# Kernel tuning notes

Measured on AMD Instinct MI355X. Metric: run time of the kernel, lower is better.

## Reference

```python
import jax, jax.numpy as jnp
import numpy as np

BATCH = 32768


def _unpack(packed, n):
    # packed: [rows, ceil(n/8)] ints in [0,256). Extract bits MSB-first per byte.
    bits = (packed[:, :, None] >> jnp.arange(7, -1, -1, dtype=packed.dtype)) & 1
    return bits.reshape(packed.shape[0], -1)[:, :n]  # [rows, n] of {0,1}


def setup_inputs() -> dict:
    key = jax.random.key(0)
    k0, k1, k2, k3, k4 = jax.random.split(key, 5)
    return {
        "x": jax.random.normal(k0, (BATCH, 784), dtype=jnp.float32),
        "w1_packed": jax.random.randint(k1, (256, 98), 0, 256, dtype=jnp.int32),
        "m1_packed": jax.random.randint(k2, (256, 98), 0, 256, dtype=jnp.int32),
        "alpha1": jnp.float32(1.0),
        "w2_packed": jax.random.randint(k3, (10, 32), 0, 256, dtype=jnp.int32),
        "m2_packed": jax.random.randint(k4, (10, 32), 0, 256, dtype=jnp.int32),
        "alpha2": jnp.float32(1.0),
    }


def reference(x, w1_packed, m1_packed, alpha1, w2_packed, m2_packed, alpha2):
    # Layer 1: binary {-1,+1} weights * {0,1} mask * alpha
    w1 = (2 * _unpack(w1_packed, 784) - 1).astype(jnp.float32)
    w1 = w1 * _unpack(m1_packed, 784).astype(jnp.float32) * alpha1  # [256, 784]
    h = jax.nn.relu(jnp.einsum('bi,oi->bo', x, w1))  # [B, 256]
    # Layer 2
    w2 = (2 * _unpack(w2_packed, 256) - 1).astype(jnp.float32)
    w2 = w2 * _unpack(m2_packed, 256).astype(jnp.float32) * alpha2  # [10, 256]
    return jnp.einsum('bh,oh->bo', h, w2)  # [B, 10]
```

## Files before the change

### kernel.cpp

```cpp
#include <hip/hip_runtime.h>
#include <hip/hip_bf16.h>

typedef __bf16 bf16x8 __attribute__((ext_vector_type(8)));
typedef float floatx4 __attribute__((ext_vector_type(4)));

__device__ __forceinline__ unsigned short f2bf(float f) {
  __bf16 b = (__bf16)f;
  return __builtin_bit_cast(unsigned short, b);
}

__global__ void decode_w1_kernel(const int* __restrict__ w1p,
                                 const int* __restrict__ m1p,
                                 unsigned short* __restrict__ w1t) {
  int t = blockIdx.x * 256 + threadIdx.x;
  int r = t & 255;
  int j = t >> 8;
  unsigned short vals[8];
#pragma unroll
  for (int k = 0; k < 8; ++k) vals[k] = 0;
  if (j < 98) {
    unsigned int v = (unsigned int)w1p[r * 98 + j];
    unsigned int m = (unsigned int)m1p[r * 98 + j];
#pragma unroll
    for (int k = 0; k < 8; ++k) {
      unsigned int bit = (v >> (7 - k)) & 1u;
      unsigned int mk  = (m >> (7 - k)) & 1u;
      vals[k] = (unsigned short)(mk ? (bit ? 0x3F80u : 0xBF80u) : 0u);
    }
  }
  uint4 pack;
  pack.x = (unsigned)vals[0] | ((unsigned)vals[1] << 16);
  pack.y = (unsigned)vals[2] | ((unsigned)vals[3] << 16);
  pack.z = (unsigned)vals[4] | ((unsigned)vals[5] << 16);
  pack.w = (unsigned)vals[6] | ((unsigned)vals[7] << 16);
  *reinterpret_cast<uint4*>(w1t + t * 8) = pack;
}

#define BM 64
#define NCHG 26
#define NCHP 13
#define HS_LD 264
#define W2_LD 264

#define OFF_W2 16896

__global__ __launch_bounds__(512, 4) void fused_kernel(
    const float* __restrict__ x,
    const unsigned short* __restrict__ w1t,
    const int* __restrict__ w2p,
    const int* __restrict__ m2p,
    const float* __restrict__ a1p,
    const float* __restrict__ a2p,
    float* __restrict__ out) {
  __shared__ unsigned short smem[26624];

  const int tid  = threadIdx.x;
  const int wave = tid >> 6;
  const int lane = tid & 63;
  const int l15  = lane & 15;
  const int quad = lane >> 4;
  const int row0 = blockIdx.x * BM;

  floatx4 acc[4][2];
#pragma unroll
  for (int i = 0; i < 4; ++i)
#pragma unroll
    for (int j = 0; j < 2; ++j) acc[i][j] = (floatx4){0.f, 0.f, 0.f, 0.f};

  const unsigned short* wl = w1t + ((size_t)wave * 32 + l15) * 8;

  auto ldfrags = [&](int cg, int cl, bf16x8* af, bf16x8* bfv) {
#pragma unroll
    for (int mi = 0; mi < 4; ++mi)
      af[mi] = *reinterpret_cast<const bf16x8*>(
          &smem[((cl * 4 + quad) * 64 + mi * 16 + l15) * 8]);
#pragma unroll
    for (int nj = 0; nj < 2; ++nj)
      bfv[nj] = *reinterpret_cast<const bf16x8*>(
          wl + (size_t)(cg * 4 + quad) * 2048 + nj * 128);
  };
  auto mm = [&](bf16x8* af, bf16x8* bfv) {
#pragma unroll
    for (int mi = 0; mi < 4; ++mi)
#pragma unroll
      for (int nj = 0; nj < 2; ++nj)
        acc[mi][nj] = __builtin_amdgcn_mfma_f32_16x16x32_bf16(
            af[mi], bfv[nj], acc[mi][nj], 0, 0, 0);
  };

  auto superphase = [&](const int sp) {
    const int r  = tid >> 3;
    const int g0 = tid & 7;
    {
      float4 xv[7];
#pragma unroll
      for (int it = 0; it < 7; ++it) {
        int g = g0 + it * 8;
        int col = sp * 416 + g * 4;
        if (col < 784)
          xv[it] = *reinterpret_cast<const float4*>(
              x + (size_t)(row0 + r) * 784 + col);
        else
          xv[it] = (float4){0.f, 0.f, 0.f, 0.f};
      }
#pragma unroll
      for (int it = 0; it < 7; ++it) {
        int g = g0 + it * 8;
        ushort4 b;
        b.x = f2bf(xv[it].x); b.y = f2bf(xv[it].y);
        b.z = f2bf(xv[it].z); b.w = f2bf(xv[it].w);
        *reinterpret_cast<ushort4*>(&smem[((g >> 1) * 64 + r) * 8 + (g & 1) * 4]) = b;
      }
    }
    {
      float4 xv[6];
#pragma unroll
      for (int it = 0; it < 6; ++it) {
        int g = g0 + 56 + it * 8;
        int col = sp * 416 + g * 4;
        if (col < 784)
          xv[it] = *reinterpret_cast<const float4*>(
              x + (size_t)(row0 + r) * 784 + col);
        else
          xv[it] = (float4){0.f, 0.f, 0.f, 0.f};
      }
#pragma unroll
      for (int it = 0; it < 6; ++it) {
        int g = g0 + 56 + it * 8;
        ushort4 b;
        b.x = f2bf(xv[it].x); b.y = f2bf(xv[it].y);
        b.z = f2bf(xv[it].z); b.w = f2bf(xv[it].w);
        *reinterpret_cast<ushort4*>(&smem[((g >> 1) * 64 + r) * 8 + (g & 1) * 4]) = b;
      }
    }
    __syncthreads();

    bf16x8 afA[4], bfA[2], afB[4], bfB[2];
    ldfrags(sp * NCHP, 0, afA, bfA);
#pragma unroll
    for (int cl = 0; cl < NCHP; ++cl) {
      if ((cl & 1) == 0) {
        if (cl < NCHP - 1) ldfrags(sp * NCHP + cl + 1, cl + 1, afB, bfB);
        mm(afA, bfA);
      } else {
        if (cl < NCHP - 1) ldfrags(sp * NCHP + cl + 1, cl + 1, afA, bfA);
        mm(afB, bfB);
      }
    }
    __syncthreads();
  };

  superphase(0);
  superphase(1);

  const float a1 = a1p[0];
  const float a2 = a2p[0];
#pragma unroll
  for (int mi = 0; mi < 4; ++mi) {
#pragma unroll
    for (int nj = 0; nj < 2; ++nj) {
      int col   = wave * 32 + nj * 16 + l15;
      int rbase = mi * 16 + quad * 4;
#pragma unroll
      for (int r = 0; r < 4; ++r) {
        float h = fmaxf(a1 * acc[mi][nj][r], 0.f);
        smem[(rbase + r) * HS_LD + col] = f2bf(h);
      }
    }
  }
  if (tid < 320) {
    int r = tid >> 5, j = tid & 31;
    unsigned int v = (unsigned int)w2p[r * 32 + j];
    unsigned int m = (unsigned int)m2p[r * 32 + j];
#pragma unroll
    for (int k = 0; k < 8; ++k) {
      unsigned int bit = (v >> (7 - k)) & 1u;
      unsigned int mk  = (m >> (7 - k)) & 1u;
      smem[OFF_W2 + r * W2_LD + j * 8 + k] =
          (unsigned short)(mk ? (bit ? 0x3F80u : 0xBF80u) : 0u);
    }
  }
  for (int idx = tid; idx < 6 * 256; idx += 512) {
    int r = 10 + (idx >> 8), c = idx & 255;
    smem[OFF_W2 + r * W2_LD + c] = 0;
  }
  __syncthreads();

  if (wave < 4) {
    floatx4 o2 = (floatx4){0.f, 0.f, 0.f, 0.f};
#pragma unroll
    for (int ks = 0; ks < 8; ++ks) {
      bf16x8 ha = *reinterpret_cast<const bf16x8*>(
          &smem[(wave * 16 + l15) * HS_LD + ks * 32 + quad * 8]);
      bf16x8 wb = *reinterpret_cast<const bf16x8*>(
          &smem[OFF_W2 + l15 * W2_LD + ks * 32 + quad * 8]);
      o2 = __builtin_amdgcn_mfma_f32_16x16x32_bf16(ha, wb, o2, 0, 0, 0);
    }
    if (l15 < 10) {
#pragma unroll
      for (int r = 0; r < 4; ++r) {
        int gr = row0 + wave * 16 + quad * 4 + r;
        out[(size_t)gr * 10 + l15] = a2 * o2[r];
      }
    }
  }
}

extern "C" void kernel_launch(void* const* d_in, const int* in_sizes, int n_in,
                              void* d_out, int out_size, void* d_ws, size_t ws_size,
                              hipStream_t stream) {
  const float* x   = (const float*)d_in[0];
  const int*   w1p = (const int*)d_in[1];
  const int*   m1p = (const int*)d_in[2];
  const float* a1  = (const float*)d_in[3];
  const int*   w2p = (const int*)d_in[4];
  const int*   m2p = (const int*)d_in[5];
  const float* a2  = (const float*)d_in[6];
  unsigned short* w1t = (unsigned short*)d_ws;
  float* out = (float*)d_out;

  decode_w1_kernel<<<104, 256, 0, stream>>>(w1p, m1p, w1t);
  fused_kernel<<<512, 512, 0, stream>>>(x, w1t, w2p, m2p, a1, a2, out);
}
```

Before: 170.9 us.

## Halve row tile to 32 and load full x row block in one pass

```diff
diff --git a/kernel.cpp b/kernel.cpp
--- a/kernel.cpp
+++ b/kernel.cpp
@@ -36,13 +36,12 @@
   *reinterpret_cast<uint4*>(w1t + t * 8) = pack;
 }
 
-#define BM 64
+#define BM 32
 #define NCHG 26
-#define NCHP 13
 #define HS_LD 264
 #define W2_LD 264
 
-#define OFF_W2 16896
+#define OFF_W2 8448
 
 __global__ __launch_bounds__(512, 4) void fused_kernel(
     const float* __restrict__ x,
@@ -61,102 +60,63 @@
   const int quad = lane >> 4;
   const int row0 = blockIdx.x * BM;
 
-  floatx4 acc[4][2];
+  {
+    const int r  = tid >> 4;
+    const int g0 = tid & 15;
+    float4 xv[13];
 #pragma unroll
-  for (int i = 0; i < 4; ++i)
+    for (int it = 0; it < 13; ++it) {
+      int g = g0 + it * 16;
+      int col = g * 4;
+      if (col < 784)
+        xv[it] = *reinterpret_cast<const float4*>(
+            x + (size_t)(row0 + r) * 784 + col);
+      else
+        xv[it] = (float4){0.f, 0.f, 0.f, 0.f};
+    }
+#pragma unroll
+    for (int it = 0; it < 13; ++it) {
+      int g = g0 + it * 16;
+      ushort4 b;
+      b.x = f2bf(xv[it].x); b.y = f2bf(xv[it].y);
+      b.z = f2bf(xv[it].z); b.w = f2bf(xv[it].w);
+      *reinterpret_cast<ushort4*>(&smem[(g >> 1) * 256 + r * 8 + (g & 1) * 4]) = b;
+    }
+  }
+  __syncthreads();
+
+  floatx4 acc[2][2];
+#pragma unroll
+  for (int i = 0; i < 2; ++i)
 #pragma unroll
     for (int j = 0; j < 2; ++j) acc[i][j] = (floatx4){0.f, 0.f, 0.f, 0.f};
 
   const unsigned short* wl = w1t + ((size_t)wave * 32 + l15) * 8;
 
-  auto ldfrags = [&](int cg, int cl, bf16x8* af, bf16x8* bfv) {
 #pragma unroll
-    for (int mi = 0; mi < 4; ++mi)
+  for (int cl = 0; cl < NCHG; ++cl) {
+    bf16x8 af[2], bfv[2];
+#pragma unroll
+    for (int mi = 0; mi < 2; ++mi)
       af[mi] = *reinterpret_cast<const bf16x8*>(
-          &smem[((cl * 4 + quad) * 64 + mi * 16 + l15) * 8]);
+          &smem[(cl * 4 + quad) * 256 + (mi * 16 + l15) * 8]);
 #pragma unroll
     for (int nj = 0; nj < 2; ++nj)
       bfv[nj] = *reinterpret_cast<const bf16x8*>(
-          wl + (size_t)(cg * 4 + quad) * 2048 + nj * 128);
-  };
-  auto mm = [&](bf16x8* af, bf16x8* bfv) {
+          wl + (size_t)(cl * 4 + quad) * 2048 + nj * 128);
 #pragma unroll
-    for (int mi = 0; mi < 4; ++mi)
+    for (int mi = 0; mi < 2; ++mi)
 #pragma unroll
       for (int nj = 0; nj < 2; ++nj)
         acc[mi][nj] = __builtin_amdgcn_mfma_f32_16x16x32_bf16(
             af[mi], bfv[nj], acc[mi][nj], 0, 0, 0);
-  };
-
-  auto superphase = [&](const int sp) {
-    const int r  = tid >> 3;
-    const int g0 = tid & 7;
-    {
-      float4 xv[7];
-#pragma unroll
-      for (int it = 0; it < 7; ++it) {
-        int g = g0 + it * 8;
-        int col = sp * 416 + g * 4;
-        if (col < 784)
-          xv[it] = *reinterpret_cast<const float4*>(
-              x + (size_t)(row0 + r) * 784 + col);
-        else
-          xv[it] = (float4){0.f, 0.f, 0.f, 0.f};
-      }
-#pragma unroll
-      for (int it = 0; it < 7; ++it) {
-        int g = g0 + it * 8;
-        ushort4 b;
-        b.x = f2bf(xv[it].x); b.y = f2bf(xv[it].y);
-        b.z = f2bf(xv[it].z); b.w = f2bf(xv[it].w);
-        *reinterpret_cast<ushort4*>(&smem[((g >> 1) * 64 + r) * 8 + (g & 1) * 4]) = b;
-      }
-    }
-    {
-      float4 xv[6];
-#pragma unroll
-      for (int it = 0; it < 6; ++it) {
-        int g = g0 + 56 + it * 8;
-        int col = sp * 416 + g * 4;
-        if (col < 784)
-          xv[it] = *reinterpret_cast<const float4*>(
-              x + (size_t)(row0 + r) * 784 + col);
-        else
-          xv[it] = (float4){0.f, 0.f, 0.f, 0.f};
-      }
-#pragma unroll
-      for (int it = 0; it < 6; ++it) {
-        int g = g0 + 56 + it * 8;
-        ushort4 b;
-        b.x = f2bf(xv[it].x); b.y = f2bf(xv[it].y);
-        b.z = f2bf(xv[it].z); b.w = f2bf(xv[it].w);
-        *reinterpret_cast<ushort4*>(&smem[((g >> 1) * 64 + r) * 8 + (g & 1) * 4]) = b;
-      }
-    }
-    __syncthreads();
-
-    bf16x8 afA[4], bfA[2], afB[4], bfB[2];
-    ldfrags(sp * NCHP, 0, afA, bfA);
-#pragma unroll
-    for (int cl = 0; cl < NCHP; ++cl) {
-      if ((cl & 1) == 0) {
-        if (cl < NCHP - 1) ldfrags(sp * NCHP + cl + 1, cl + 1, afB, bfB);
-        mm(afA, bfA);
-      } else {
-        if (cl < NCHP - 1) ldfrags(sp * NCHP + cl + 1, cl + 1, afA, bfA);
-        mm(afB, bfB);
-      }
-    }
-    __syncthreads();
-  };
-
-  superphase(0);
-  superphase(1);
+  }
+  __syncthreads();
 
   const float a1 = a1p[0];
   const float a2 = a2p[0];
 #pragma unroll
-  for (int mi = 0; mi < 4; ++mi) {
+  for (int mi = 0; mi < 2; ++mi) {
 #pragma unroll
     for (int nj = 0; nj < 2; ++nj) {
       int col   = wave * 32 + nj * 16 + l15;
@@ -186,7 +146,7 @@
   }
   __syncthreads();
 
-  if (wave < 4) {
+  if (wave < 2) {
     floatx4 o2 = (floatx4){0.f, 0.f, 0.f, 0.f};
 #pragma unroll
     for (int ks = 0; ks < 8; ++ks) {
@@ -220,5 +180,5 @@
   float* out = (float*)d_out;
 
   decode_w1_kernel<<<104, 256, 0, stream>>>(w1p, m1p, w1t);
-  fused_kernel<<<512, 512, 0, stream>>>(x, w1t, w2p, m2p, a1, a2, out);
+  fused_kernel<<<1024, 512, 0, stream>>>(x, w1t, w2p, m2p, a1, a2, out);
 }
```

After: 172.4 us. About the same (+0.9%).

## Overlap second-half x loads with first-half MFMA compute in fused MLP kernel

Applied to the files above, without the earlier changes.

```diff
diff --git a/kernel.cpp b/kernel.cpp
--- a/kernel.cpp
+++ b/kernel.cpp
@@ -37,8 +37,6 @@
 }
 
 #define BM 64
-#define NCHG 26
-#define NCHP 13
 #define HS_LD 264
 #define W2_LD 264
 
@@ -69,89 +67,108 @@
 
   const unsigned short* wl = w1t + ((size_t)wave * 32 + l15) * 8;
 
-  auto ldfrags = [&](int cg, int cl, bf16x8* af, bf16x8* bfv) {
+  const int r  = tid >> 3;
+  const int g0 = tid & 7;
+  const float* xrow = x + (size_t)(row0 + r) * 784;
+
+  bf16x8 bfv[2][2];
+  auto pref_w = [&](int cg, int buf) {
+#pragma unroll
+    for (int nj = 0; nj < 2; ++nj)
+      bfv[buf][nj] = *reinterpret_cast<const bf16x8*>(
+          wl + (size_t)(cg * 4 + quad) * 2048 + nj * 128);
+  };
+  auto mm = [&](int cl, int buf) {
+    bf16x8 af[4];
 #pragma unroll
     for (int mi = 0; mi < 4; ++mi)
       af[mi] = *reinterpret_cast<const bf16x8*>(
           &smem[((cl * 4 + quad) * 64 + mi * 16 + l15) * 8]);
 #pragma unroll
-    for (int nj = 0; nj < 2; ++nj)
-      bfv[nj] = *reinterpret_cast<const bf16x8*>(
-          wl + (size_t)(cg * 4 + quad) * 2048 + nj * 128);
-  };
-  auto mm = [&](bf16x8* af, bf16x8* bfv) {
-#pragma unroll
     for (int mi = 0; mi < 4; ++mi)
 #pragma unroll
       for (int nj = 0; nj < 2; ++nj)
         acc[mi][nj] = __builtin_amdgcn_mfma_f32_16x16x32_bf16(
-            af[mi], bfv[nj], acc[mi][nj], 0, 0, 0);
+            af[mi], bfv[buf][nj], acc[mi][nj], 0, 0, 0);
   };
 
-  auto superphase = [&](const int sp) {
-    const int r  = tid >> 3;
-    const int g0 = tid & 7;
-    {
-      float4 xv[7];
-#pragma unroll
-      for (int it = 0; it < 7; ++it) {
-        int g = g0 + it * 8;
-        int col = sp * 416 + g * 4;
-        if (col < 784)
-          xv[it] = *reinterpret_cast<const float4*>(
-              x + (size_t)(row0 + r) * 784 + col);
-        else
-          xv[it] = (float4){0.f, 0.f, 0.f, 0.f};
-      }
-#pragma unroll
-      for (int it = 0; it < 7; ++it) {
-        int g = g0 + it * 8;
-        ushort4 b;
-        b.x = f2bf(xv[it].x); b.y = f2bf(xv[it].y);
-        b.z = f2bf(xv[it].z); b.w = f2bf(xv[it].w);
-        *reinterpret_cast<ushort4*>(&smem[((g >> 1) * 64 + r) * 8 + (g & 1) * 4]) = b;
-      }
-    }
-    {
-      float4 xv[6];
-#pragma unroll
-      for (int it = 0; it < 6; ++it) {
-        int g = g0 + 56 + it * 8;
-        int col = sp * 416 + g * 4;
-        if (col < 784)
-          xv[it] = *reinterpret_cast<const float4*>(
-              x + (size_t)(row0 + r) * 784 + col);
-        else
-          xv[it] = (float4){0.f, 0.f, 0.f, 0.f};
-      }
-#pragma unroll
-      for (int it = 0; it < 6; ++it) {
-        int g = g0 + 56 + it * 8;
-        ushort4 b;
-        b.x = f2bf(xv[it].x); b.y = f2bf(xv[it].y);
-        b.z = f2bf(xv[it].z); b.w = f2bf(xv[it].w);
-        *reinterpret_cast<ushort4*>(&smem[((g >> 1) * 64 + r) * 8 + (g & 1) * 4]) = b;
-      }
-    }
-    __syncthreads();
-
-    bf16x8 afA[4], bfA[2], afB[4], bfB[2];
-    ldfrags(sp * NCHP, 0, afA, bfA);
-#pragma unroll
-    for (int cl = 0; cl < NCHP; ++cl) {
-      if ((cl & 1) == 0) {
-        if (cl < NCHP - 1) ldfrags(sp * NCHP + cl + 1, cl + 1, afB, bfB);
-        mm(afA, bfA);
-      } else {
-        if (cl < NCHP - 1) ldfrags(sp * NCHP + cl + 1, cl + 1, afA, bfA);
-        mm(afB, bfB);
-      }
-    }
-    __syncthreads();
-  };
-
-  superphase(0);
-  superphase(1);
+  {
+    float4 xv[13];
+#pragma unroll
+    for (int it = 0; it < 13; ++it) {
+      int g = g0 + it * 8;
+      xv[it] = *reinterpret_cast<const float4*>(xrow + g * 4);
+    }
+#pragma unroll
+    for (int it = 0; it < 13; ++it) {
+      int g = g0 + it * 8;
+      ushort4 b;
+      b.x = f2bf(xv[it].x); b.y = f2bf(xv[it].y);
+      b.z = f2bf(xv[it].z); b.w = f2bf(xv[it].w);
+      *reinterpret_cast<ushort4*>(&smem[((g >> 1) * 64 + r) * 8 + (g & 1) * 4]) = b;
+    }
+  }
+  __syncthreads();
+
+  float4 xvA[7];
+#pragma unroll
+  for (int it = 0; it < 7; ++it) {
+    int g = 104 + g0 + it * 8;
+    xvA[it] = *reinterpret_cast<const float4*>(xrow + g * 4);
+  }
+
+  pref_w(0, 0);
+#pragma unroll
+  for (int cl = 0; cl < 6; ++cl) {
+    pref_w(cl + 1, (cl + 1) & 1);
+    mm(cl, cl & 1);
+  }
+
+  ushort4 xsA[7];
+#pragma unroll
+  for (int it = 0; it < 7; ++it) {
+    xsA[it].x = f2bf(xvA[it].x); xsA[it].y = f2bf(xvA[it].y);
+    xsA[it].z = f2bf(xvA[it].z); xsA[it].w = f2bf(xvA[it].w);
+  }
+  float4 xvB[6];
+#pragma unroll
+  for (int it = 0; it < 6; ++it) {
+    int g = 104 + g0 + (7 + it) * 8;
+    if (g * 4 < 784)
+      xvB[it] = *reinterpret_cast<const float4*>(xrow + g * 4);
+    else
+      xvB[it] = (float4){0.f, 0.f, 0.f, 0.f};
+  }
+
+#pragma unroll
+  for (int cl = 6; cl < 13; ++cl) {
+    if (cl < 12) pref_w(cl + 1, (cl + 1) & 1);
+    mm(cl, cl & 1);
+  }
+  __syncthreads();
+
+#pragma unroll
+  for (int it = 0; it < 7; ++it) {
+    int lg = g0 + it * 8;
+    *reinterpret_cast<ushort4*>(&smem[((lg >> 1) * 64 + r) * 8 + (lg & 1) * 4]) = xsA[it];
+  }
+#pragma unroll
+  for (int it = 0; it < 6; ++it) {
+    int lg = g0 + (7 + it) * 8;
+    ushort4 b;
+    b.x = f2bf(xvB[it].x); b.y = f2bf(xvB[it].y);
+    b.z = f2bf(xvB[it].z); b.w = f2bf(xvB[it].w);
+    *reinterpret_cast<ushort4*>(&smem[((lg >> 1) * 64 + r) * 8 + (lg & 1) * 4]) = b;
+  }
+  __syncthreads();
+
+  pref_w(13, 0);
+#pragma unroll
+  for (int cl = 0; cl < 13; ++cl) {
+    if (cl < 12) pref_w(13 + cl + 1, (cl + 1) & 1);
+    mm(cl, cl & 1);
+  }
+  __syncthreads();
 
   const float a1 = a1p[0];
   const float a2 = a2p[0];
@@ -162,27 +179,27 @@
       int col   = wave * 32 + nj * 16 + l15;
       int rbase = mi * 16 + quad * 4;
 #pragma unroll
-      for (int r = 0; r < 4; ++r) {
-        float h = fmaxf(a1 * acc[mi][nj][r], 0.f);
-        smem[(rbase + r) * HS_LD + col] = f2bf(h);
+      for (int rr = 0; rr < 4; ++rr) {
+        float h = fmaxf(a1 * acc[mi][nj][rr], 0.f);
+        smem[(rbase + rr) * HS_LD + col] = f2bf(h);
       }
     }
   }
   if (tid < 320) {
-    int r = tid >> 5, j = tid & 31;
-    unsigned int v = (unsigned int)w2p[r * 32 + j];
-    unsigned int m = (unsigned int)m2p[r * 32 + j];
+    int rr = tid >> 5, j = tid & 31;
+    unsigned int v = (unsigned int)w2p[rr * 32 + j];
+    unsigned int m = (unsigned int)m2p[rr * 32 + j];
 #pragma unroll
     for (int k = 0; k < 8; ++k) {
       unsigned int bit = (v >> (7 - k)) & 1u;
       unsigned int mk  = (m >> (7 - k)) & 1u;
-      smem[OFF_W2 + r * W2_LD + j * 8 + k] =
+      smem[OFF_W2 + rr * W2_LD + j * 8 + k] =
           (unsigned short)(mk ? (bit ? 0x3F80u : 0xBF80u) : 0u);
     }
   }
   for (int idx = tid; idx < 6 * 256; idx += 512) {
-    int r = 10 + (idx >> 8), c = idx & 255;
-    smem[OFF_W2 + r * W2_LD + c] = 0;
+    int rr = 10 + (idx >> 8), c = idx & 255;
+    smem[OFF_W2 + rr * W2_LD + c] = 0;
   }
   __syncthreads();
 
@@ -198,9 +215,9 @@
     }
     if (l15 < 10) {
 #pragma unroll
-      for (int r = 0; r < 4; ++r) {
-        int gr = row0 + wave * 16 + quad * 4 + r;
-        out[(size_t)gr * 10 + l15] = a2 * o2[r];
+      for (int rr = 0; rr < 4; ++rr) {
+        int gr = row0 + wave * 16 + quad * 4 + rr;
+        out[(size_t)gr * 10 + l15] = a2 * o2[rr];
       }
     }
   }
```

Measured after the change: 169.4 us. No clear change (-0.9%).
